# Kernel tuning notes

Hardware: AMD Instinct MI355X
Metric: run time of the kernel (lower is better)

The kernel has to match this reference:

```python
import jax, jax.numpy as jnp
import numpy as np

N, E = 50000, 800000          # n_nodes, n_edges
IN_C, OUT_C = 128, 64         # in_channels, out_channels


def setup_inputs() -> dict:
    key = jax.random.key(0)
    ks = jax.random.split(key, 12)
    def w(k, i, o):
        return jax.random.normal(k, (i, o), jnp.float32) / np.float32(np.sqrt(i))
    return {
        "x": jax.random.normal(ks[0], (N, IN_C), jnp.float32),
        "edge_index": jax.random.randint(ks[1], (2, E), 0, N),
        "eps": jax.random.normal(ks[2], (N, OUT_C), jnp.float32),
        # encoder GCNConv1: in -> 2*out
        "W_e1": w(ks[3], IN_C, 2 * OUT_C), "b_e1": jnp.zeros((2 * OUT_C,), jnp.float32),
        # encoder GCNConv2: 2*out -> out
        "W_e2": w(ks[4], 2 * OUT_C, OUT_C), "b_e2": jnp.zeros((OUT_C,), jnp.float32),
        # fc_mu / fc_logvar: out -> out
        "W_mu": w(ks[5], OUT_C, OUT_C), "b_mu": jnp.zeros((OUT_C,), jnp.float32),
        "W_lv": w(ks[6], OUT_C, OUT_C), "b_lv": jnp.zeros((OUT_C,), jnp.float32),
        # decoder GCNConv1: out -> in
        "W_d1": w(ks[7], OUT_C, IN_C), "b_d1": jnp.zeros((IN_C,), jnp.float32),
        # decoder GCNConv2: in -> in
        "W_d2": w(ks[8], IN_C, IN_C), "b_d2": jnp.zeros((IN_C,), jnp.float32),
    }


def _gcn_norm(edge_index, n):
    # PyG gcn_norm: add self-loops, symmetric D^-1/2 A D^-1/2 normalization
    loop = jnp.arange(n)
    src = jnp.concatenate([edge_index[0], loop])
    dst = jnp.concatenate([edge_index[1], loop])
    deg = jax.ops.segment_sum(jnp.ones_like(dst, jnp.float32), dst, num_segments=n)
    dinv = jnp.where(deg > 0, deg ** -0.5, 0.0)
    norm = dinv[src] * dinv[dst]  # [E + N]
    return src, dst, norm


def _gcn_conv(x, W, b, src, dst, norm, n):
    h = x @ W                       # linear transform first (small channel dim)
    msg = h[src] * norm[:, None]    # gather + edge scaling
    return jax.ops.segment_sum(msg, dst, num_segments=n) + b  # scatter-add + bias


def reference(x, edge_index, eps, W_e1, b_e1, W_e2, b_e2, W_mu, b_mu, W_lv, b_lv, W_d1, b_d1, W_d2, b_d2):
    n = x.shape[0]
    src, dst, norm = _gcn_norm(edge_index, n)
    # encoder
    h = jax.nn.relu(_gcn_conv(x, W_e1, b_e1, src, dst, norm, n))
    h = _gcn_conv(h, W_e2, b_e2, src, dst, norm, n)
    mu = h @ W_mu + b_mu
    logvar = h @ W_lv + b_lv
    # reparameterize (training mode)
    z = mu + eps * jnp.exp(0.5 * logvar)
    # decoder
    d = jax.nn.relu(_gcn_conv(z, W_d1, b_d1, src, dst, norm, n))
    d = _gcn_conv(d, W_d2, b_d2, src, dst, norm, n)
    return (d, mu, logvar)
```

## Files before the change

### kernel.cpp

```cpp
#include <hip/hip_runtime.h>
#include <math.h>

typedef unsigned short u16;
typedef unsigned int u32;
typedef __attribute__((ext_vector_type(8))) short s16x8;
typedef __attribute__((ext_vector_type(4))) float f32x4;

__device__ __forceinline__ float bf2f(u16 u) { return __uint_as_float(((u32)u) << 16); }
__device__ __forceinline__ u16 f2bf(float f) {
    u32 u = __float_as_uint(f);
    return (u16)((u + 0x7fffu + ((u >> 16) & 1u)) >> 16);
}

union U4 { u32 u[4]; s16x8 v; };

__device__ __forceinline__ s16x8 pack_hi(f32x4 x0, f32x4 x1) {
    U4 r;
    r.u[0] = (__float_as_uint(x0.y) & 0xFFFF0000u) | (__float_as_uint(x0.x) >> 16);
    r.u[1] = (__float_as_uint(x0.w) & 0xFFFF0000u) | (__float_as_uint(x0.z) >> 16);
    r.u[2] = (__float_as_uint(x1.y) & 0xFFFF0000u) | (__float_as_uint(x1.x) >> 16);
    r.u[3] = (__float_as_uint(x1.w) & 0xFFFF0000u) | (__float_as_uint(x1.z) >> 16);
    return r.v;
}
__device__ __forceinline__ s16x8 pack_lo(f32x4 x0, f32x4 x1) {
    float e0 = x0.x - __uint_as_float(__float_as_uint(x0.x) & 0xFFFF0000u);
    float e1 = x0.y - __uint_as_float(__float_as_uint(x0.y) & 0xFFFF0000u);
    float e2 = x0.z - __uint_as_float(__float_as_uint(x0.z) & 0xFFFF0000u);
    float e3 = x0.w - __uint_as_float(__float_as_uint(x0.w) & 0xFFFF0000u);
    float e4 = x1.x - __uint_as_float(__float_as_uint(x1.x) & 0xFFFF0000u);
    float e5 = x1.y - __uint_as_float(__float_as_uint(x1.y) & 0xFFFF0000u);
    float e6 = x1.z - __uint_as_float(__float_as_uint(x1.z) & 0xFFFF0000u);
    float e7 = x1.w - __uint_as_float(__float_as_uint(x1.w) & 0xFFFF0000u);
    U4 r;
    r.u[0] = (__float_as_uint(e1) & 0xFFFF0000u) | (__float_as_uint(e0) >> 16);
    r.u[1] = (__float_as_uint(e3) & 0xFFFF0000u) | (__float_as_uint(e2) >> 16);
    r.u[2] = (__float_as_uint(e5) & 0xFFFF0000u) | (__float_as_uint(e4) >> 16);
    r.u[3] = (__float_as_uint(e7) & 0xFFFF0000u) | (__float_as_uint(e6) >> 16);
    return r.v;
}

#define BSHIFT 9
#define BSIZE 512
#define BCAP 10240


struct PackArgs { const float* w[6]; };

__global__ __launch_bounds__(256) void k_pack6(PackArgs pa, u16* __restrict__ out) {
    const int Ks[6] = {128, 128, 64, 64, 64, 128};
    const int Ms[6] = {128, 64, 64, 64, 128, 128};
    const int Off[6] = {0, 16384, 24576, 28672, 32768, 40960};
    int s = blockIdx.y;
    int K = Ks[s], M = Ms[s];
    int id = blockIdx.x * 256 + threadIdx.x;
    if (id >= K * M) return;
    int ms = (M == 128) ? 7 : 6;
    int k = id >> ms, c = id & (M - 1);
    int chunk = k >> 5, j = k & 7, lq = (k >> 3) & 3;
    int ct = c >> 4, ln = (c & 15) + (lq << 4);
    out[Off[s] + (chunk * (M >> 4) + ct) * 512 + ln * 8 + j] = f2bf(pa.w[s][id]);
}


__global__ __launch_bounds__(256) void k_bin(const int* __restrict__ ei, int E, int NB,
                                             int* __restrict__ bin_cursor, u32* __restrict__ binned) {
    __shared__ int hist[128];
    __shared__ int base_l[128];
    const int t = threadIdx.x;
    const int e0 = blockIdx.x * 4096;
    int sreg[16], dreg[16];
#pragma unroll
    for (int j = 0; j < 16; ++j) {
        int e = e0 + j * 256 + t;
        if (e < E) {
            sreg[j] = ei[e];
            dreg[j] = ei[E + e];
        } else {
            dreg[j] = -1;
        }
    }
    if (t < NB) hist[t] = 0;
    __syncthreads();
#pragma unroll
    for (int j = 0; j < 16; ++j)
        if (dreg[j] >= 0) atomicAdd(&hist[dreg[j] >> BSHIFT], 1);
    __syncthreads();
    if (t < NB) {
        base_l[t] = atomicAdd(&bin_cursor[t], hist[t]);
        hist[t] = 0;
    }
    __syncthreads();
#pragma unroll
    for (int j = 0; j < 16; ++j)
        if (dreg[j] >= 0) {
            int b = dreg[j] >> BSHIFT;
            int pos = base_l[b] + atomicAdd(&hist[b], 1);
            if (pos < BCAP) binned[(size_t)b * BCAP + pos] = ((u32)(dreg[j] & (BSIZE - 1)) << 17) | (u32)sreg[j];
        }
}


__global__ __launch_bounds__(256) void k_cnt_alloc(const u32* __restrict__ binned,
                                                   const int* __restrict__ bin_cursor, int N,
                                                   int* __restrict__ cnt, float* __restrict__ dinv,
                                                   int* __restrict__ row_start, int* __restrict__ cursor) {
    __shared__ int cnt_l[BSIZE];
    __shared__ int wave_sum[5];
    __shared__ int base_s;
    const int t = threadIdx.x;
    const int b = blockIdx.x;
    const int lane = t & 63, w = t >> 6;
    cnt_l[t] = 0;
    cnt_l[t + 256] = 0;
    __syncthreads();
    const int n = min(bin_cursor[b], BCAP);
    for (int i = t; i < n; i += 256) atomicAdd(&cnt_l[binned[(size_t)b * BCAP + i] >> 17], 1);
    __syncthreads();
    int c0 = cnt_l[2 * t], c1 = cnt_l[2 * t + 1];
    int p0 = (c0 + 7) & ~7, p1 = (c1 + 7) & ~7;
    int s = p0 + p1;
    int incl = s;
#pragma unroll
    for (int o = 1; o < 64; o <<= 1) {
        int v = __shfl_up(incl, o, 64);
        if (lane >= o) incl += v;
    }
    if (lane == 63) wave_sum[w] = incl;
    __syncthreads();
    if (t == 0) {
        int acc = 0;
#pragma unroll
        for (int i = 0; i < 4; ++i) {
            int v = wave_sum[i];
            wave_sum[i] = acc;
            acc += v;
        }
        base_s = atomicAdd(cursor, acc);
    }
    __syncthreads();
    int excl = incl - s + wave_sum[w] + base_s;
    int v0 = b * BSIZE + 2 * t;
    if (v0 < N) {
        cnt[v0] = c0;
        dinv[v0] = rsqrtf((float)(c0 + 1));
        row_start[v0] = excl;
    }
    if (v0 + 1 < N) {
        cnt[v0 + 1] = c1;
        dinv[v0 + 1] = rsqrtf((float)(c1 + 1));
        row_start[v0 + 1] = excl + p0;
    }
}


__global__ __launch_bounds__(256) void k_scatter(const u32* __restrict__ binned,
                                                 const int* __restrict__ bin_cursor,
                                                 const int* __restrict__ row_start, const int* __restrict__ cnt,
                                                 const float* __restrict__ dinv, int N,
                                                 int2* __restrict__ edges) {
    __shared__ float dv_l[BSIZE];
    __shared__ int rs_l[BSIZE];
    __shared__ int fill_l[BSIZE];
    const int t = threadIdx.x;
    const int b = blockIdx.x;
#pragma unroll
    for (int hh = 0; hh < 2; ++hh) {
        int d = t + hh * 256;
        int v = b * BSIZE + d;
        bool ok = v < N;
        dv_l[d] = ok ? dinv[v] : 0.f;
        rs_l[d] = ok ? row_start[v] : 0;
        fill_l[d] = 0;
    }
    __syncthreads();
    const int n = min(bin_cursor[b], BCAP);
    for (int i = t; i < n; i += 256) {
        u32 e = binned[(size_t)b * BCAP + i];
        int dl = e >> 17;
        int src = e & 0x1FFFF;
        float wgt = dinv[src] * dv_l[dl];
        int pos = rs_l[dl] + atomicAdd(&fill_l[dl], 1);
        edges[pos] = make_int2(src, __float_as_int(wgt));
    }
    __syncthreads();
#pragma unroll
    for (int hh = 0; hh < 2; ++hh) {
        int d = t + hh * 256;
        int v = b * BSIZE + d;
        if (v >= N) continue;
        int c = fill_l[d];
        int pc = (c + 7) & ~7;
        for (int j = c; j < pc; ++j) edges[rs_l[d] + j] = make_int2(0, 0);
    }
}


template <int K, int M, int RT, int NSET, bool XBF16, bool OUT_BF16, bool BREL>
__global__ __launch_bounds__(256, 3) void k_gemm(const void* __restrict__ Xv, const u16* __restrict__ Bpk,
                                                 const float* __restrict__ b0, const float* __restrict__ b1,
                                                 const float* __restrict__ eps,
                                                 void* __restrict__ Y0, float* __restrict__ Y1,
                                                 u16* __restrict__ Z, int N) {
    constexpr int CH = K / 32;
    constexpr int TPM = M >> 4;
    constexpr int SETSTRIDE = CH * TPM * 512;
    const int lane = threadIdx.x & 63, w = threadIdx.x >> 6;
    const int l15 = lane & 15, q = lane >> 4;
    const int col0 = blockIdx.x * 64;
    const int row0 = blockIdx.y * (RT * 64);

    s16x8 Bfr[NSET * CH * 4];
#pragma unroll
    for (int s = 0; s < NSET; ++s)
#pragma unroll
        for (int ch = 0; ch < CH; ++ch)
#pragma unroll
            for (int ct = 0; ct < 4; ++ct)
                Bfr[(s * CH + ch) * 4 + ct] =
                    *(const s16x8*)&Bpk[(size_t)s * SETSTRIDE + ((ch * TPM) + (col0 >> 4) + ct) * 512 + lane * 8];

    f32x4 acc[NSET][RT][4];
#pragma unroll
    for (int s = 0; s < NSET; ++s)
#pragma unroll
        for (int rt = 0; rt < RT; ++rt)
#pragma unroll
            for (int ct = 0; ct < 4; ++ct) acc[s][rt][ct] = 0.f;

#pragma unroll
    for (int ch = 0; ch < CH; ++ch) {
#pragma unroll
        for (int rt = 0; rt < RT; ++rt) {
            int r = row0 + (w * RT + rt) * 16 + l15;
            r = r < N ? r : N - 1;
            s16x8 ah, al;
            if (XBF16) {
                ah = *(const s16x8*)((const u16*)Xv + (size_t)r * K + (ch << 5) + (q << 3));
            } else {
                const float* xp = (const float*)Xv + (size_t)r * K + (ch << 5) + (q << 3);
                f32x4 x0 = *(const f32x4*)xp;
                f32x4 x1 = *(const f32x4*)(xp + 4);
                ah = pack_hi(x0, x1);
                al = pack_lo(x0, x1);
            }
#pragma unroll
            for (int s = 0; s < NSET; ++s)
#pragma unroll
                for (int ct = 0; ct < 4; ++ct) {
                    int fb = (s * CH + ch) * 4 + ct;
                    acc[s][rt][ct] = __builtin_amdgcn_mfma_f32_16x16x32_bf16(ah, Bfr[fb], acc[s][rt][ct], 0, 0, 0);
                    if (!XBF16)
                        acc[s][rt][ct] = __builtin_amdgcn_mfma_f32_16x16x32_bf16(al, Bfr[fb], acc[s][rt][ct], 0, 0, 0);
                }
        }
    }

#pragma unroll
    for (int rt = 0; rt < RT; ++rt)
#pragma unroll
        for (int ct = 0; ct < 4; ++ct)
#pragma unroll
            for (int reg = 0; reg < 4; ++reg) {
                int row = row0 + (w * RT + rt) * 16 + q * 4 + reg;
                if (row >= N) continue;
                int col = col0 + ct * 16 + l15;
                if (NSET == 1) {
                    float v = acc[0][rt][ct][reg];
                    if (BREL) v = fmaxf(v + b0[col], 0.f);
                    if (OUT_BF16)
                        ((u16*)Y0)[(size_t)row * M + col] = f2bf(v);
                    else
                        ((float*)Y0)[(size_t)row * M + col] = v;
                } else {
                    float mu = acc[0][rt][ct][reg] + b0[col];
                    float lv = acc[1][rt][ct][reg] + b1[col];
                    size_t o = (size_t)row * 64 + col;
                    ((float*)Y0)[o] = mu;
                    Y1[o] = lv;
                    Z[o] = f2bf(mu + eps[o] * expf(0.5f * lv));
                }
            }
}


template <bool RELU, bool OUT_BF16>
__global__ __launch_bounds__(256) void k_agg128(const u16* __restrict__ hin, const int2* __restrict__ edges,
                                                const int* __restrict__ row_start, const int* __restrict__ cnt,
                                                const float* __restrict__ dinv, const float* __restrict__ bias,
                                                void* __restrict__ out, int N) {
    const int v = blockIdx.x * 4 + (threadIdx.x >> 6);
    const int lane = threadIdx.x & 63;
    if (v >= N) return;
    const int start = __builtin_amdgcn_readfirstlane(row_start[v]);
    const int c = __builtin_amdgcn_readfirstlane(cnt[v]);
    const int pc = (c + 7) & ~7;
    const u32* hp = (const u32*)hin;
    float a0 = 0.f, a1 = 0.f;
    if (pc) {
        int2 e[8];
#pragma unroll
        for (int j = 0; j < 8; ++j) e[j] = edges[start + j];
        for (int i = 0; i < pc; i += 8) {
            u32 h[8];
            float wv[8];
#pragma unroll
            for (int j = 0; j < 8; ++j) {
                h[j] = hp[(size_t)e[j].x * 64 + lane];
                wv[j] = __int_as_float(e[j].y);
            }
            if (i + 8 < pc) {
#pragma unroll
                for (int j = 0; j < 8; ++j) e[j] = edges[start + i + 8 + j];
            }
#pragma unroll
            for (int j = 0; j < 8; ++j) {
                a0 = fmaf(wv[j], bf2f((u16)h[j]), a0);
                a1 = fmaf(wv[j], bf2f((u16)(h[j] >> 16)), a1);
            }
        }
    }
    float dv = dinv[v], sw = dv * dv;
    u32 hs = hp[(size_t)v * 64 + lane];
    a0 = fmaf(sw, bf2f((u16)hs), a0);
    a1 = fmaf(sw, bf2f((u16)(hs >> 16)), a1);
    float2 bp = ((const float2*)bias)[lane];
    a0 += bp.x;
    a1 += bp.y;
    if (RELU) { a0 = fmaxf(a0, 0.f); a1 = fmaxf(a1, 0.f); }
    if (OUT_BF16)
        ((u32*)out)[(size_t)v * 64 + lane] = (u32)f2bf(a0) | ((u32)f2bf(a1) << 16);
    else
        ((float2*)out)[(size_t)v * 64 + lane] = make_float2(a0, a1);
}

template <bool HASB>
__global__ __launch_bounds__(256) void k_agg64(const u16* __restrict__ hin, const int2* __restrict__ edges,
                                               const int* __restrict__ row_start, const int* __restrict__ cnt,
                                               const float* __restrict__ dinv, const float* __restrict__ bias,
                                               float* __restrict__ out, int N) {
    const int v = blockIdx.x * 4 + (threadIdx.x >> 6);
    const int lane = threadIdx.x & 63;
    if (v >= N) return;
    const int start = __builtin_amdgcn_readfirstlane(row_start[v]);
    const int c = __builtin_amdgcn_readfirstlane(cnt[v]);
    const int pc = (c + 7) & ~7;
    float a0 = 0.f;
    if (pc) {
        int2 e[8];
#pragma unroll
        for (int j = 0; j < 8; ++j) e[j] = edges[start + j];
        for (int i = 0; i < pc; i += 8) {
            u16 h[8];
            float wv[8];
#pragma unroll
            for (int j = 0; j < 8; ++j) {
                h[j] = hin[(size_t)e[j].x * 64 + lane];
                wv[j] = __int_as_float(e[j].y);
            }
            if (i + 8 < pc) {
#pragma unroll
                for (int j = 0; j < 8; ++j) e[j] = edges[start + i + 8 + j];
            }
#pragma unroll
            for (int j = 0; j < 8; ++j) a0 = fmaf(wv[j], bf2f(h[j]), a0);
        }
    }
    float dv = dinv[v];
    a0 = fmaf(dv * dv, bf2f(hin[(size_t)v * 64 + lane]), a0);
    if (HASB) a0 += bias[lane];
    out[(size_t)v * 64 + lane] = a0;
}


extern "C" void kernel_launch(void* const* d_in, const int* in_sizes, int n_in,
                              void* d_out, int out_size, void* d_ws, size_t ws_size,
                              hipStream_t stream) {
    const float* x = (const float*)d_in[0];
    const int* ei = (const int*)d_in[1];
    const float* eps = (const float*)d_in[2];
    const float* We1 = (const float*)d_in[3];
    const float* be1 = (const float*)d_in[4];
    const float* We2 = (const float*)d_in[5];
    const float* be2 = (const float*)d_in[6];
    const float* Wmu = (const float*)d_in[7];
    const float* bmu = (const float*)d_in[8];
    const float* Wlv = (const float*)d_in[9];
    const float* blv = (const float*)d_in[10];
    const float* Wd1 = (const float*)d_in[11];
    const float* bd1 = (const float*)d_in[12];
    const float* Wd2 = (const float*)d_in[13];
    const float* bd2 = (const float*)d_in[14];

    const int N = in_sizes[0] / 128;
    const int E = in_sizes[1] / 2;
    const int ECAP = E + 8 * N;
    const int NB = (N + BSIZE - 1) >> BSHIFT;

    int* bin_cursor = (int*)d_ws;
    int* cursor = bin_cursor + 128;
    float* dinv = (float*)(bin_cursor + 256);
    int* row_start = (int*)(dinv + N);
    int* cnt = row_start + N;
    int2* edges = (int2*)(cnt + N);
    u16* R1 = (u16*)(edges + ECAP);
    u16* AZu = R1 + (size_t)N * 128;
    float* AZf = (float*)AZu;
    u32* binned = (u32*)AZu;
    u16* Wpk = AZu + (size_t)N * 128;

    float* out_d = (float*)d_out;
    float* out_mu = out_d + (size_t)N * 128;
    float* out_lv = out_mu + (size_t)N * 64;
    float* H2 = out_d;

    hipMemsetAsync(d_ws, 0, 256 * 4, stream);

    PackArgs pa;
    pa.w[0] = We1; pa.w[1] = We2; pa.w[2] = Wmu; pa.w[3] = Wlv; pa.w[4] = Wd1; pa.w[5] = Wd2;
    k_pack6<<<dim3(64, 6), dim3(256), 0, stream>>>(pa, Wpk);

    k_bin<<<dim3((E + 4095) / 4096), dim3(256), 0, stream>>>(ei, E, NB, bin_cursor, binned);
    k_cnt_alloc<<<dim3(NB), dim3(256), 0, stream>>>(binned, bin_cursor, N, cnt, dinv, row_start, cursor);
    k_scatter<<<dim3(NB), dim3(256), 0, stream>>>(binned, bin_cursor, row_start, cnt, dinv, N, edges);

    const int RB128 = (N + 127) / 128;
    const int RB64 = (N + 63) / 64;
    const int AB = (N + 3) / 4;

    k_gemm<128, 128, 2, 1, false, true, false><<<dim3(2, RB128), dim3(256), 0, stream>>>(x, Wpk, nullptr, nullptr, nullptr, R1, nullptr, nullptr, N);
    k_agg128<true, true><<<dim3(AB), dim3(256), 0, stream>>>(R1, edges, row_start, cnt, dinv, be1, AZu, N);
    k_gemm<128, 64, 1, 1, true, true, false><<<dim3(1, RB64), dim3(256), 0, stream>>>(AZu, Wpk + 16384, nullptr, nullptr, nullptr, R1, nullptr, nullptr, N);
    k_agg64<true><<<dim3(AB), dim3(256), 0, stream>>>(R1, edges, row_start, cnt, dinv, be2, H2, N);
    k_gemm<64, 64, 1, 2, false, false, false><<<dim3(1, RB64), dim3(256), 0, stream>>>(H2, Wpk + 24576, bmu, blv, eps, out_mu, out_lv, R1, N);
    k_agg64<false><<<dim3(AB), dim3(256), 0, stream>>>(R1, edges, row_start, cnt, dinv, nullptr, AZf, N);
    k_gemm<64, 128, 2, 1, false, true, true><<<dim3(2, RB128), dim3(256), 0, stream>>>(AZf, Wpk + 32768, bd1, nullptr, nullptr, AZu, nullptr, nullptr, N);
    k_gemm<128, 128, 2, 1, true, true, false><<<dim3(2, RB128), dim3(256), 0, stream>>>(AZu, Wpk + 40960, nullptr, nullptr, nullptr, R1, nullptr, nullptr, N);
    k_agg128<false, false><<<dim3(AB), dim3(256), 0, stream>>>(R1, edges, row_start, cnt, dinv, bd2, out_d, N);
}
```

Baseline: 338.8 us.

## Fuse all GCN VAE phases into one persistent cooperative kernel with grid syncs

Replaces the sequence of separate launches (pack, bin, count, scatter, GEMMs, aggregations) with a single cooperative persistent kernel that loops over work tiles and separates phases with grid-wide syncs. The first GEMM runs alongside edge binning on the blocks not used for binning. Edge row padding and the aggregation unroll grow from 8 to 16 so each load batch covers more neighbours. This removes per-launch overhead and the memset, at the cost of grid-sync barriers, a grid capped by occupancy, and extra padded edges.

```diff
diff --git a/kernel.cpp b/kernel.cpp
--- a/kernel.cpp
+++ b/kernel.cpp
@@ -1,5 +1,8 @@
 #include <hip/hip_runtime.h>
+#include <hip/hip_cooperative_groups.h>
 #include <math.h>
+
+namespace cg = cooperative_groups;
 
 typedef unsigned short u16;
 typedef unsigned int u32;
@@ -43,50 +46,63 @@
 #define BSIZE 512
 #define BCAP 10240
 
-
-struct PackArgs { const float* w[6]; };
-
-__global__ __launch_bounds__(256) void k_pack6(PackArgs pa, u16* __restrict__ out) {
+struct MegaArgs {
+    const float* x;
+    const int* ei;
+    const float* eps;
+    const float* w[6];
+    const float* be1; const float* be2; const float* bmu;
+    const float* blv; const float* bd1; const float* bd2;
+    int* bin_cursor; int* cursor;
+    float* dinv; int* row_start; int* cnt;
+    int2* edges;
+    u16* R1; u16* AZu; u16* B2; u32* binned; u16* Wpk;
+    float* out_d; float* out_mu; float* out_lv;
+    int N, E, NB;
+};
+
+
+__device__ __forceinline__ void ph_pack(const MegaArgs& A, int G, int bid, int t) {
+    if (bid == 0 && t < 256) A.bin_cursor[t] = 0;
     const int Ks[6] = {128, 128, 64, 64, 64, 128};
     const int Ms[6] = {128, 64, 64, 64, 128, 128};
     const int Off[6] = {0, 16384, 24576, 28672, 32768, 40960};
-    int s = blockIdx.y;
-    int K = Ks[s], M = Ms[s];
-    int id = blockIdx.x * 256 + threadIdx.x;
-    if (id >= K * M) return;
-    int ms = (M == 128) ? 7 : 6;
-    int k = id >> ms, c = id & (M - 1);
-    int chunk = k >> 5, j = k & 7, lq = (k >> 3) & 3;
-    int ct = c >> 4, ln = (c & 15) + (lq << 4);
-    out[Off[s] + (chunk * (M >> 4) + ct) * 512 + ln * 8 + j] = f2bf(pa.w[s][id]);
-}
-
-
-__global__ __launch_bounds__(256) void k_bin(const int* __restrict__ ei, int E, int NB,
-                                             int* __restrict__ bin_cursor, u32* __restrict__ binned) {
-    __shared__ int hist[128];
-    __shared__ int base_l[128];
-    const int t = threadIdx.x;
-    const int e0 = blockIdx.x * 4096;
+    for (int g = bid; g < 384; g += G) {
+        int s = g >> 6;
+        int id = (g & 63) * 256 + t;
+        int K = Ks[s], M = Ms[s];
+        if (id < K * M) {
+            int ms = (M == 128) ? 7 : 6;
+            int k = id >> ms, c = id & (M - 1);
+            int chunk = k >> 5, j = k & 7, lq = (k >> 3) & 3;
+            int ct = c >> 4, ln = (c & 15) + (lq << 4);
+            A.Wpk[Off[s] + (chunk * (M >> 4) + ct) * 512 + ln * 8 + j] = f2bf(A.w[s][id]);
+        }
+    }
+}
+
+
+__device__ __forceinline__ void ph_bin(const MegaArgs& A, int c, int t, int* hist, int* base_l) {
+    const int e0 = c * 4096;
     int sreg[16], dreg[16];
 #pragma unroll
     for (int j = 0; j < 16; ++j) {
         int e = e0 + j * 256 + t;
-        if (e < E) {
-            sreg[j] = ei[e];
-            dreg[j] = ei[E + e];
+        if (e < A.E) {
+            sreg[j] = A.ei[e];
+            dreg[j] = A.ei[A.E + e];
         } else {
             dreg[j] = -1;
         }
     }
-    if (t < NB) hist[t] = 0;
+    if (t < A.NB) hist[t] = 0;
     __syncthreads();
 #pragma unroll
     for (int j = 0; j < 16; ++j)
         if (dreg[j] >= 0) atomicAdd(&hist[dreg[j] >> BSHIFT], 1);
     __syncthreads();
-    if (t < NB) {
-        base_l[t] = atomicAdd(&bin_cursor[t], hist[t]);
+    if (t < A.NB) {
+        base_l[t] = atomicAdd(&A.bin_cursor[t], hist[t]);
         hist[t] = 0;
     }
     __syncthreads();
@@ -95,29 +111,21 @@
         if (dreg[j] >= 0) {
             int b = dreg[j] >> BSHIFT;
             int pos = base_l[b] + atomicAdd(&hist[b], 1);
-            if (pos < BCAP) binned[(size_t)b * BCAP + pos] = ((u32)(dreg[j] & (BSIZE - 1)) << 17) | (u32)sreg[j];
-        }
-}
-
-
-__global__ __launch_bounds__(256) void k_cnt_alloc(const u32* __restrict__ binned,
-                                                   const int* __restrict__ bin_cursor, int N,
-                                                   int* __restrict__ cnt, float* __restrict__ dinv,
-                                                   int* __restrict__ row_start, int* __restrict__ cursor) {
-    __shared__ int cnt_l[BSIZE];
-    __shared__ int wave_sum[5];
-    __shared__ int base_s;
-    const int t = threadIdx.x;
-    const int b = blockIdx.x;
+            if (pos < BCAP) A.binned[(size_t)b * BCAP + pos] = ((u32)(dreg[j] & (BSIZE - 1)) << 17) | (u32)sreg[j];
+        }
+}
+
+
+__device__ __forceinline__ void ph_cnt(const MegaArgs& A, int b, int t, int* cnt_l, int* wave_sum, int* base_s) {
     const int lane = t & 63, w = t >> 6;
     cnt_l[t] = 0;
     cnt_l[t + 256] = 0;
     __syncthreads();
-    const int n = min(bin_cursor[b], BCAP);
-    for (int i = t; i < n; i += 256) atomicAdd(&cnt_l[binned[(size_t)b * BCAP + i] >> 17], 1);
+    const int n = min(A.bin_cursor[b], BCAP);
+    for (int i = t; i < n; i += 256) atomicAdd(&cnt_l[A.binned[(size_t)b * BCAP + i] >> 17], 1);
     __syncthreads();
     int c0 = cnt_l[2 * t], c1 = cnt_l[2 * t + 1];
-    int p0 = (c0 + 7) & ~7, p1 = (c1 + 7) & ~7;
+    int p0 = (c0 + 15) & ~15, p1 = (c1 + 15) & ~15;
     int s = p0 + p1;
     int incl = s;
 #pragma unroll
@@ -135,265 +143,300 @@
             wave_sum[i] = acc;
             acc += v;
         }
-        base_s = atomicAdd(cursor, acc);
-    }
-    __syncthreads();
-    int excl = incl - s + wave_sum[w] + base_s;
+        *base_s = atomicAdd(A.cursor, acc);
+    }
+    __syncthreads();
+    int excl = incl - s + wave_sum[w] + *base_s;
     int v0 = b * BSIZE + 2 * t;
-    if (v0 < N) {
-        cnt[v0] = c0;
-        dinv[v0] = rsqrtf((float)(c0 + 1));
-        row_start[v0] = excl;
-    }
-    if (v0 + 1 < N) {
-        cnt[v0 + 1] = c1;
-        dinv[v0 + 1] = rsqrtf((float)(c1 + 1));
-        row_start[v0 + 1] = excl + p0;
-    }
-}
-
-
-__global__ __launch_bounds__(256) void k_scatter(const u32* __restrict__ binned,
-                                                 const int* __restrict__ bin_cursor,
-                                                 const int* __restrict__ row_start, const int* __restrict__ cnt,
-                                                 const float* __restrict__ dinv, int N,
-                                                 int2* __restrict__ edges) {
-    __shared__ float dv_l[BSIZE];
-    __shared__ int rs_l[BSIZE];
-    __shared__ int fill_l[BSIZE];
-    const int t = threadIdx.x;
-    const int b = blockIdx.x;
+    if (v0 < A.N) {
+        A.cnt[v0] = c0;
+        A.dinv[v0] = rsqrtf((float)(c0 + 1));
+        A.row_start[v0] = excl;
+    }
+    if (v0 + 1 < A.N) {
+        A.cnt[v0 + 1] = c1;
+        A.dinv[v0 + 1] = rsqrtf((float)(c1 + 1));
+        A.row_start[v0 + 1] = excl + p0;
+    }
+}
+
+
+__device__ __forceinline__ void ph_scatter(const MegaArgs& A, int b, int t, float* dv_l, int* rs_l, int* fill_l) {
 #pragma unroll
     for (int hh = 0; hh < 2; ++hh) {
         int d = t + hh * 256;
         int v = b * BSIZE + d;
-        bool ok = v < N;
-        dv_l[d] = ok ? dinv[v] : 0.f;
-        rs_l[d] = ok ? row_start[v] : 0;
+        bool ok = v < A.N;
+        dv_l[d] = ok ? A.dinv[v] : 0.f;
+        rs_l[d] = ok ? A.row_start[v] : 0;
         fill_l[d] = 0;
     }
     __syncthreads();
-    const int n = min(bin_cursor[b], BCAP);
+    const int n = min(A.bin_cursor[b], BCAP);
     for (int i = t; i < n; i += 256) {
-        u32 e = binned[(size_t)b * BCAP + i];
+        u32 e = A.binned[(size_t)b * BCAP + i];
         int dl = e >> 17;
         int src = e & 0x1FFFF;
-        float wgt = dinv[src] * dv_l[dl];
+        float wgt = A.dinv[src] * dv_l[dl];
         int pos = rs_l[dl] + atomicAdd(&fill_l[dl], 1);
-        edges[pos] = make_int2(src, __float_as_int(wgt));
+        A.edges[pos] = make_int2(src, __float_as_int(wgt));
     }
     __syncthreads();
 #pragma unroll
     for (int hh = 0; hh < 2; ++hh) {
         int d = t + hh * 256;
         int v = b * BSIZE + d;
-        if (v >= N) continue;
+        if (v >= A.N) continue;
         int c = fill_l[d];
-        int pc = (c + 7) & ~7;
-        for (int j = c; j < pc; ++j) edges[rs_l[d] + j] = make_int2(0, 0);
-    }
-}
-
-
-template <int K, int M, int RT, int NSET, bool XBF16, bool OUT_BF16, bool BREL>
-__global__ __launch_bounds__(256, 3) void k_gemm(const void* __restrict__ Xv, const u16* __restrict__ Bpk,
-                                                 const float* __restrict__ b0, const float* __restrict__ b1,
-                                                 const float* __restrict__ eps,
-                                                 void* __restrict__ Y0, float* __restrict__ Y1,
-                                                 u16* __restrict__ Z, int N) {
+        int pc = (c + 15) & ~15;
+        for (int j = c; j < pc; ++j) A.edges[rs_l[d] + j] = make_int2(0, 0);
+    }
+}
+
+
+template <int K, int M, int RT, int NSET, int CB, bool XBF16, bool OUT_BF16, bool BREL>
+__device__ void ph_gemm(const void* __restrict__ Xv, const u16* __restrict__ Bpk,
+                        const float* __restrict__ b0, const float* __restrict__ b1,
+                        const float* __restrict__ eps, void* __restrict__ Y0,
+                        float* __restrict__ Y1, u16* __restrict__ Z, int N, int RB,
+                        int G, int bid, int t) {
     constexpr int CH = K / 32;
     constexpr int TPM = M >> 4;
     constexpr int SETSTRIDE = CH * TPM * 512;
-    const int lane = threadIdx.x & 63, w = threadIdx.x >> 6;
+    const int lane = t & 63, w = t >> 6;
     const int l15 = lane & 15, q = lane >> 4;
-    const int col0 = blockIdx.x * 64;
-    const int row0 = blockIdx.y * (RT * 64);
-
-    s16x8 Bfr[NSET * CH * 4];
-#pragma unroll
-    for (int s = 0; s < NSET; ++s)
-#pragma unroll
-        for (int ch = 0; ch < CH; ++ch)
+    for (int tt = bid; tt < CB * RB; tt += G) {
+        const int col0 = (CB == 2) ? ((tt & 1) * 64) : 0;
+        const int row0 = ((CB == 2) ? (tt >> 1) : tt) * (RT * 64);
+
+        s16x8 Bfr[NSET * CH * 4];
+#pragma unroll
+        for (int s = 0; s < NSET; ++s)
+#pragma unroll
+            for (int ch = 0; ch < CH; ++ch)
+#pragma unroll
+                for (int ct = 0; ct < 4; ++ct)
+                    Bfr[(s * CH + ch) * 4 + ct] =
+                        *(const s16x8*)&Bpk[(size_t)s * SETSTRIDE + ((ch * TPM) + (col0 >> 4) + ct) * 512 + lane * 8];
+
+        f32x4 acc[NSET][RT][4];
+#pragma unroll
+        for (int s = 0; s < NSET; ++s)
+#pragma unroll
+            for (int rt = 0; rt < RT; ++rt)
+#pragma unroll
+                for (int ct = 0; ct < 4; ++ct) acc[s][rt][ct] = 0.f;
+
+#pragma unroll
+        for (int ch = 0; ch < CH; ++ch) {
+#pragma unroll
+            for (int rt = 0; rt < RT; ++rt) {
+                int r = row0 + (w * RT + rt) * 16 + l15;
+                r = r < N ? r : N - 1;
+                s16x8 ah, al;
+                if (XBF16) {
+                    ah = *(const s16x8*)((const u16*)Xv + (size_t)r * K + (ch << 5) + (q << 3));
+                } else {
+                    const float* xp = (const float*)Xv + (size_t)r * K + (ch << 5) + (q << 3);
+                    f32x4 x0 = *(const f32x4*)xp;
+                    f32x4 x1 = *(const f32x4*)(xp + 4);
+                    ah = pack_hi(x0, x1);
+                    al = pack_lo(x0, x1);
+                }
+#pragma unroll
+                for (int s = 0; s < NSET; ++s)
+#pragma unroll
+                    for (int ct = 0; ct < 4; ++ct) {
+                        int fb = (s * CH + ch) * 4 + ct;
+                        acc[s][rt][ct] = __builtin_amdgcn_mfma_f32_16x16x32_bf16(ah, Bfr[fb], acc[s][rt][ct], 0, 0, 0);
+                        if (!XBF16)
+                            acc[s][rt][ct] = __builtin_amdgcn_mfma_f32_16x16x32_bf16(al, Bfr[fb], acc[s][rt][ct], 0, 0, 0);
+                    }
+            }
+        }
+
+#pragma unroll
+        for (int rt = 0; rt < RT; ++rt)
 #pragma unroll
             for (int ct = 0; ct < 4; ++ct)
-                Bfr[(s * CH + ch) * 4 + ct] =
-                    *(const s16x8*)&Bpk[(size_t)s * SETSTRIDE + ((ch * TPM) + (col0 >> 4) + ct) * 512 + lane * 8];
-
-    f32x4 acc[NSET][RT][4];
-#pragma unroll
-    for (int s = 0; s < NSET; ++s)
-#pragma unroll
-        for (int rt = 0; rt < RT; ++rt)
-#pragma unroll
-            for (int ct = 0; ct < 4; ++ct) acc[s][rt][ct] = 0.f;
-
-#pragma unroll
-    for (int ch = 0; ch < CH; ++ch) {
-#pragma unroll
-        for (int rt = 0; rt < RT; ++rt) {
-            int r = row0 + (w * RT + rt) * 16 + l15;
-            r = r < N ? r : N - 1;
-            s16x8 ah, al;
-            if (XBF16) {
-                ah = *(const s16x8*)((const u16*)Xv + (size_t)r * K + (ch << 5) + (q << 3));
-            } else {
-                const float* xp = (const float*)Xv + (size_t)r * K + (ch << 5) + (q << 3);
-                f32x4 x0 = *(const f32x4*)xp;
-                f32x4 x1 = *(const f32x4*)(xp + 4);
-                ah = pack_hi(x0, x1);
-                al = pack_lo(x0, x1);
+#pragma unroll
+                for (int reg = 0; reg < 4; ++reg) {
+                    int row = row0 + (w * RT + rt) * 16 + q * 4 + reg;
+                    if (row >= N) continue;
+                    int col = col0 + ct * 16 + l15;
+                    if (NSET == 1) {
+                        float v = acc[0][rt][ct][reg];
+                        if (BREL) v = fmaxf(v + b0[col], 0.f);
+                        if (OUT_BF16)
+                            ((u16*)Y0)[(size_t)row * M + col] = f2bf(v);
+                        else
+                            ((float*)Y0)[(size_t)row * M + col] = v;
+                    } else {
+                        float mu = acc[0][rt][ct][reg] + b0[col];
+                        float lv = acc[1][rt][ct][reg] + b1[col];
+                        size_t o = (size_t)row * 64 + col;
+                        ((float*)Y0)[o] = mu;
+                        Y1[o] = lv;
+                        Z[o] = f2bf(mu + eps[o] * expf(0.5f * lv));
+                    }
+                }
+    }
+}
+
+
+template <bool RELU, bool OUT_BF16>
+__device__ void ph_agg128(const MegaArgs& A, const u16* __restrict__ hin, const float* __restrict__ bias,
+                          void* __restrict__ out, int G, int bid, int t) {
+    const int w = t >> 6, lane = t & 63;
+    const int AB = (A.N + 3) >> 2;
+    const u32* hp = (const u32*)hin;
+    for (int g = bid; g < AB; g += G) {
+        const int v = g * 4 + w;
+        if (v >= A.N) continue;
+        const int start = __builtin_amdgcn_readfirstlane(A.row_start[v]);
+        const int c = __builtin_amdgcn_readfirstlane(A.cnt[v]);
+        const int pc = (c + 15) & ~15;
+        float a0 = 0.f, a1 = 0.f;
+        if (pc) {
+            int2 e[16];
+#pragma unroll
+            for (int j = 0; j < 16; ++j) e[j] = A.edges[start + j];
+            for (int i = 0; i < pc; i += 16) {
+                u32 h[16];
+                float wv[16];
+#pragma unroll
+                for (int j = 0; j < 16; ++j) {
+                    h[j] = hp[(size_t)e[j].x * 64 + lane];
+                    wv[j] = __int_as_float(e[j].y);
+                }
+                if (i + 16 < pc) {
+#pragma unroll
+                    for (int j = 0; j < 16; ++j) e[j] = A.edges[start + i + 16 + j];
+                }
+#pragma unroll
+                for (int j = 0; j < 16; ++j) {
+                    a0 = fmaf(wv[j], bf2f((u16)h[j]), a0);
+                    a1 = fmaf(wv[j], bf2f((u16)(h[j] >> 16)), a1);
+                }
             }
-#pragma unroll
-            for (int s = 0; s < NSET; ++s)
-#pragma unroll
-                for (int ct = 0; ct < 4; ++ct) {
-                    int fb = (s * CH + ch) * 4 + ct;
-                    acc[s][rt][ct] = __builtin_amdgcn_mfma_f32_16x16x32_bf16(ah, Bfr[fb], acc[s][rt][ct], 0, 0, 0);
-                    if (!XBF16)
-                        acc[s][rt][ct] = __builtin_amdgcn_mfma_f32_16x16x32_bf16(al, Bfr[fb], acc[s][rt][ct], 0, 0, 0);
-                }
-        }
-    }
-
-#pragma unroll
-    for (int rt = 0; rt < RT; ++rt)
-#pragma unroll
-        for (int ct = 0; ct < 4; ++ct)
-#pragma unroll
-            for (int reg = 0; reg < 4; ++reg) {
-                int row = row0 + (w * RT + rt) * 16 + q * 4 + reg;
-                if (row >= N) continue;
-                int col = col0 + ct * 16 + l15;
-                if (NSET == 1) {
-                    float v = acc[0][rt][ct][reg];
-                    if (BREL) v = fmaxf(v + b0[col], 0.f);
-                    if (OUT_BF16)
-                        ((u16*)Y0)[(size_t)row * M + col] = f2bf(v);
-                    else
-                        ((float*)Y0)[(size_t)row * M + col] = v;
-                } else {
-                    float mu = acc[0][rt][ct][reg] + b0[col];
-                    float lv = acc[1][rt][ct][reg] + b1[col];
-                    size_t o = (size_t)row * 64 + col;
-                    ((float*)Y0)[o] = mu;
-                    Y1[o] = lv;
-                    Z[o] = f2bf(mu + eps[o] * expf(0.5f * lv));
-                }
+        }
+        float dv = A.dinv[v], sw = dv * dv;
+        u32 hs = hp[(size_t)v * 64 + lane];
+        a0 = fmaf(sw, bf2f((u16)hs), a0);
+        a1 = fmaf(sw, bf2f((u16)(hs >> 16)), a1);
+        float2 bp = ((const float2*)bias)[lane];
+        a0 += bp.x;
+        a1 += bp.y;
+        if (RELU) { a0 = fmaxf(a0, 0.f); a1 = fmaxf(a1, 0.f); }
+        if (OUT_BF16)
+            ((u32*)out)[(size_t)v * 64 + lane] = (u32)f2bf(a0) | ((u32)f2bf(a1) << 16);
+        else
+            ((float2*)out)[(size_t)v * 64 + lane] = make_float2(a0, a1);
+    }
+}
+
+template <bool HASB>
+__device__ void ph_agg64(const MegaArgs& A, const u16* __restrict__ hin, const float* __restrict__ bias,
+                         float* __restrict__ out, int G, int bid, int t) {
+    const int w = t >> 6, lane = t & 63;
+    const int AB = (A.N + 3) >> 2;
+    for (int g = bid; g < AB; g += G) {
+        const int v = g * 4 + w;
+        if (v >= A.N) continue;
+        const int start = __builtin_amdgcn_readfirstlane(A.row_start[v]);
+        const int c = __builtin_amdgcn_readfirstlane(A.cnt[v]);
+        const int pc = (c + 15) & ~15;
+        float a0 = 0.f;
+        if (pc) {
+            int2 e[16];
+#pragma unroll
+            for (int j = 0; j < 16; ++j) e[j] = A.edges[start + j];
+            for (int i = 0; i < pc; i += 16) {
+                u16 h[16];
+                float wv[16];
+#pragma unroll
+                for (int j = 0; j < 16; ++j) {
+                    h[j] = hin[(size_t)e[j].x * 64 + lane];
+                    wv[j] = __int_as_float(e[j].y);
+                }
+                if (i + 16 < pc) {
+#pragma unroll
+                    for (int j = 0; j < 16; ++j) e[j] = A.edges[start + i + 16 + j];
+                }
+#pragma unroll
+                for (int j = 0; j < 16; ++j) a0 = fmaf(wv[j], bf2f(h[j]), a0);
             }
-}
-
-
-template <bool RELU, bool OUT_BF16>
-__global__ __launch_bounds__(256) void k_agg128(const u16* __restrict__ hin, const int2* __restrict__ edges,
-                                                const int* __restrict__ row_start, const int* __restrict__ cnt,
-                                                const float* __restrict__ dinv, const float* __restrict__ bias,
-                                                void* __restrict__ out, int N) {
-    const int v = blockIdx.x * 4 + (threadIdx.x >> 6);
-    const int lane = threadIdx.x & 63;
-    if (v >= N) return;
-    const int start = __builtin_amdgcn_readfirstlane(row_start[v]);
-    const int c = __builtin_amdgcn_readfirstlane(cnt[v]);
-    const int pc = (c + 7) & ~7;
-    const u32* hp = (const u32*)hin;
-    float a0 = 0.f, a1 = 0.f;
-    if (pc) {
-        int2 e[8];
-#pragma unroll
-        for (int j = 0; j < 8; ++j) e[j] = edges[start + j];
-        for (int i = 0; i < pc; i += 8) {
-            u32 h[8];
-            float wv[8];
-#pragma unroll
-            for (int j = 0; j < 8; ++j) {
-                h[j] = hp[(size_t)e[j].x * 64 + lane];
-                wv[j] = __int_as_float(e[j].y);
-            }
-            if (i + 8 < pc) {
-#pragma unroll
-                for (int j = 0; j < 8; ++j) e[j] = edges[start + i + 8 + j];
-            }
-#pragma unroll
-            for (int j = 0; j < 8; ++j) {
-                a0 = fmaf(wv[j], bf2f((u16)h[j]), a0);
-                a1 = fmaf(wv[j], bf2f((u16)(h[j] >> 16)), a1);
-            }
-        }
-    }
-    float dv = dinv[v], sw = dv * dv;
-    u32 hs = hp[(size_t)v * 64 + lane];
-    a0 = fmaf(sw, bf2f((u16)hs), a0);
-    a1 = fmaf(sw, bf2f((u16)(hs >> 16)), a1);
-    float2 bp = ((const float2*)bias)[lane];
-    a0 += bp.x;
-    a1 += bp.y;
-    if (RELU) { a0 = fmaxf(a0, 0.f); a1 = fmaxf(a1, 0.f); }
-    if (OUT_BF16)
-        ((u32*)out)[(size_t)v * 64 + lane] = (u32)f2bf(a0) | ((u32)f2bf(a1) << 16);
-    else
-        ((float2*)out)[(size_t)v * 64 + lane] = make_float2(a0, a1);
-}
-
-template <bool HASB>
-__global__ __launch_bounds__(256) void k_agg64(const u16* __restrict__ hin, const int2* __restrict__ edges,
-                                               const int* __restrict__ row_start, const int* __restrict__ cnt,
-                                               const float* __restrict__ dinv, const float* __restrict__ bias,
-                                               float* __restrict__ out, int N) {
-    const int v = blockIdx.x * 4 + (threadIdx.x >> 6);
-    const int lane = threadIdx.x & 63;
-    if (v >= N) return;
-    const int start = __builtin_amdgcn_readfirstlane(row_start[v]);
-    const int c = __builtin_amdgcn_readfirstlane(cnt[v]);
-    const int pc = (c + 7) & ~7;
-    float a0 = 0.f;
-    if (pc) {
-        int2 e[8];
-#pragma unroll
-        for (int j = 0; j < 8; ++j) e[j] = edges[start + j];
-        for (int i = 0; i < pc; i += 8) {
-            u16 h[8];
-            float wv[8];
-#pragma unroll
-            for (int j = 0; j < 8; ++j) {
-                h[j] = hin[(size_t)e[j].x * 64 + lane];
-                wv[j] = __int_as_float(e[j].y);
-            }
-            if (i + 8 < pc) {
-#pragma unroll
-                for (int j = 0; j < 8; ++j) e[j] = edges[start + i + 8 + j];
-            }
-#pragma unroll
-            for (int j = 0; j < 8; ++j) a0 = fmaf(wv[j], bf2f(h[j]), a0);
-        }
-    }
-    float dv = dinv[v];
-    a0 = fmaf(dv * dv, bf2f(hin[(size_t)v * 64 + lane]), a0);
-    if (HASB) a0 += bias[lane];
-    out[(size_t)v * 64 + lane] = a0;
+        }
+        float dv = A.dinv[v];
+        a0 = fmaf(dv * dv, bf2f(hin[(size_t)v * 64 + lane]), a0);
+        if (HASB) a0 += bias[lane];
+        out[(size_t)v * 64 + lane] = a0;
+    }
+}
+
+
+__global__ __launch_bounds__(256, 3) void k_mega(MegaArgs A) {
+    const int G = gridDim.x, bid = blockIdx.x, t = threadIdx.x;
+    __shared__ alignas(16) int smem[1600];
+    cg::grid_group gg = cg::this_grid();
+
+    const int RB128 = (A.N + 127) >> 7;
+    const int RB64 = (A.N + 63) >> 6;
+
+    ph_pack(A, G, bid, t);
+    gg.sync();
+
+    {
+        const int C = (A.E + 4095) >> 12;
+        if (bid < C)
+            ph_bin(A, bid, t, smem, smem + 128);
+        else
+            ph_gemm<128, 128, 2, 1, 2, false, true, false>(A.x, A.Wpk, nullptr, nullptr, nullptr,
+                                                           A.R1, nullptr, nullptr, A.N, RB128, G - C, bid - C, t);
+    }
+    gg.sync();
+
+    if (bid < A.NB) ph_cnt(A, bid, t, smem, smem + 512, smem + 520);
+    gg.sync();
+
+    if (bid < A.NB) ph_scatter(A, bid, t, (float*)smem, smem + 512, smem + 1024);
+    gg.sync();
+
+    ph_agg128<true, true>(A, A.R1, A.be1, A.AZu, G, bid, t);
+    gg.sync();
+
+    ph_gemm<128, 64, 1, 1, 1, true, true, false>(A.AZu, A.Wpk + 16384, nullptr, nullptr, nullptr,
+                                                 A.R1, nullptr, nullptr, A.N, RB64, G, bid, t);
+    gg.sync();
+
+    ph_agg64<true>(A, A.R1, A.be2, A.out_d, G, bid, t);
+    gg.sync();
+
+    ph_gemm<64, 64, 1, 2, 1, false, false, false>(A.out_d, A.Wpk + 24576, A.bmu, A.blv, A.eps,
+                                                  A.out_mu, A.out_lv, A.R1, A.N, RB64, G, bid, t);
+    gg.sync();
+
+    ph_agg64<false>(A, A.R1, nullptr, (float*)A.AZu, G, bid, t);
+    gg.sync();
+
+    ph_gemm<64, 128, 2, 1, 2, false, true, true>((const float*)A.AZu, A.Wpk + 32768, A.bd1, nullptr, nullptr,
+                                                 A.B2, nullptr, nullptr, A.N, RB128, G, bid, t);
+    gg.sync();
+
+    ph_gemm<128, 128, 2, 1, 2, true, true, false>(A.B2, A.Wpk + 40960, nullptr, nullptr, nullptr,
+                                                  A.R1, nullptr, nullptr, A.N, RB128, G, bid, t);
+    gg.sync();
+
+    ph_agg128<false, false>(A, A.R1, A.bd2, A.out_d, G, bid, t);
 }
 
 
 extern "C" void kernel_launch(void* const* d_in, const int* in_sizes, int n_in,
                               void* d_out, int out_size, void* d_ws, size_t ws_size,
                               hipStream_t stream) {
-    const float* x = (const float*)d_in[0];
-    const int* ei = (const int*)d_in[1];
-    const float* eps = (const float*)d_in[2];
-    const float* We1 = (const float*)d_in[3];
-    const float* be1 = (const float*)d_in[4];
-    const float* We2 = (const float*)d_in[5];
-    const float* be2 = (const float*)d_in[6];
-    const float* Wmu = (const float*)d_in[7];
-    const float* bmu = (const float*)d_in[8];
-    const float* Wlv = (const float*)d_in[9];
-    const float* blv = (const float*)d_in[10];
-    const float* Wd1 = (const float*)d_in[11];
-    const float* bd1 = (const float*)d_in[12];
-    const float* Wd2 = (const float*)d_in[13];
-    const float* bd2 = (const float*)d_in[14];
-
     const int N = in_sizes[0] / 128;
     const int E = in_sizes[1] / 2;
-    const int ECAP = E + 8 * N;
+    const int ECAP = E + 16 * N;
     const int NB = (N + BSIZE - 1) >> BSHIFT;
 
     int* bin_cursor = (int*)d_ws;
@@ -404,36 +447,59 @@
     int2* edges = (int2*)(cnt + N);
     u16* R1 = (u16*)(edges + ECAP);
     u16* AZu = R1 + (size_t)N * 128;
-    float* AZf = (float*)AZu;
+    u16* B2 = AZu + (size_t)N * 128;
+    u16* Wpk = B2 + (size_t)N * 128;
     u32* binned = (u32*)AZu;
-    u16* Wpk = AZu + (size_t)N * 128;
 
     float* out_d = (float*)d_out;
     float* out_mu = out_d + (size_t)N * 128;
     float* out_lv = out_mu + (size_t)N * 64;
-    float* H2 = out_d;
-
-    hipMemsetAsync(d_ws, 0, 256 * 4, stream);
-
-    PackArgs pa;
-    pa.w[0] = We1; pa.w[1] = We2; pa.w[2] = Wmu; pa.w[3] = Wlv; pa.w[4] = Wd1; pa.w[5] = Wd2;
-    k_pack6<<<dim3(64, 6), dim3(256), 0, stream>>>(pa, Wpk);
-
-    k_bin<<<dim3((E + 4095) / 4096), dim3(256), 0, stream>>>(ei, E, NB, bin_cursor, binned);
-    k_cnt_alloc<<<dim3(NB), dim3(256), 0, stream>>>(binned, bin_cursor, N, cnt, dinv, row_start, cursor);
-    k_scatter<<<dim3(NB), dim3(256), 0, stream>>>(binned, bin_cursor, row_start, cnt, dinv, N, edges);
-
-    const int RB128 = (N + 127) / 128;
-    const int RB64 = (N + 63) / 64;
-    const int AB = (N + 3) / 4;
-
-    k_gemm<128, 128, 2, 1, false, true, false><<<dim3(2, RB128), dim3(256), 0, stream>>>(x, Wpk, nullptr, nullptr, nullptr, R1, nullptr, nullptr, N);
-    k_agg128<true, true><<<dim3(AB), dim3(256), 0, stream>>>(R1, edges, row_start, cnt, dinv, be1, AZu, N);
-    k_gemm<128, 64, 1, 1, true, true, false><<<dim3(1, RB64), dim3(256), 0, stream>>>(AZu, Wpk + 16384, nullptr, nullptr, nullptr, R1, nullptr, nullptr, N);
-    k_agg64<true><<<dim3(AB), dim3(256), 0, stream>>>(R1, edges, row_start, cnt, dinv, be2, H2, N);
-    k_gemm<64, 64, 1, 2, false, false, false><<<dim3(1, RB64), dim3(256), 0, stream>>>(H2, Wpk + 24576, bmu, blv, eps, out_mu, out_lv, R1, N);
-    k_agg64<false><<<dim3(AB), dim3(256), 0, stream>>>(R1, edges, row_start, cnt, dinv, nullptr, AZf, N);
-    k_gemm<64, 128, 2, 1, false, true, true><<<dim3(2, RB128), dim3(256), 0, stream>>>(AZf, Wpk + 32768, bd1, nullptr, nullptr, AZu, nullptr, nullptr, N);
-    k_gemm<128, 128, 2, 1, true, true, false><<<dim3(2, RB128), dim3(256), 0, stream>>>(AZu, Wpk + 40960, nullptr, nullptr, nullptr, R1, nullptr, nullptr, N);
-    k_agg128<false, false><<<dim3(AB), dim3(256), 0, stream>>>(R1, edges, row_start, cnt, dinv, bd2, out_d, N);
-}
+
+    MegaArgs A;
+    A.x = (const float*)d_in[0];
+    A.ei = (const int*)d_in[1];
+    A.eps = (const float*)d_in[2];
+    A.w[0] = (const float*)d_in[3];
+    A.be1 = (const float*)d_in[4];
+    A.w[1] = (const float*)d_in[5];
+    A.be2 = (const float*)d_in[6];
+    A.w[2] = (const float*)d_in[7];
+    A.bmu = (const float*)d_in[8];
+    A.w[3] = (const float*)d_in[9];
+    A.blv = (const float*)d_in[10];
+    A.w[4] = (const float*)d_in[11];
+    A.bd1 = (const float*)d_in[12];
+    A.w[5] = (const float*)d_in[13];
+    A.bd2 = (const float*)d_in[14];
+    A.bin_cursor = bin_cursor;
+    A.cursor = cursor;
+    A.dinv = dinv;
+    A.row_start = row_start;
+    A.cnt = cnt;
+    A.edges = edges;
+    A.R1 = R1;
+    A.AZu = AZu;
+    A.B2 = B2;
+    A.binned = binned;
+    A.Wpk = Wpk;
+    A.out_d = out_d;
+    A.out_mu = out_mu;
+    A.out_lv = out_lv;
+    A.N = N;
+    A.E = E;
+    A.NB = NB;
+
+    static int nblk = 0;
+    if (nblk == 0) {
+        hipDeviceProp_t prop{};
+        hipGetDeviceProperties(&prop, 0);
+        int bpc = 0;
+        hipOccupancyMaxActiveBlocksPerMultiprocessor(&bpc, reinterpret_cast<const void*>(k_mega), 256, 0);
+        if (bpc < 1) bpc = 1;
+        int cu = prop.multiProcessorCount > 0 ? prop.multiProcessorCount : 256;
+        nblk = cu * bpc;
+    }
+
+    void* args[] = {(void*)&A};
+    hipLaunchCooperativeKernel(reinterpret_cast<const void*>(k_mega), dim3(nblk), dim3(256), args, 0, stream);
+}
```

Result: slower. 961.9 us (+183.9%).
